# Performance work log

Hardware: AMD Instinct MI355X
Metric: run time of the kernel (lower is better)

## Reference

```python
import jax, jax.numpy as jnp
import numpy as np

B, T, D = 4, 512, 512
NB, NH, PF, K = 2, 8, 2, 4
INNER = PF * D          # 1024
DH = INNER // NH        # 128
NC = 1000
EPS = 1e-5


def _ln(x, s, b):
    mu = x.mean(-1, keepdims=True)
    var = x.var(-1, keepdims=True)
    return (x - mu) / jnp.sqrt(var + EPS) * s + b


def _causal_conv(x, k, b):
    # x: [B,T,C], depthwise kernel k: [C,K]
    kk = k.shape[-1]
    xp = jnp.pad(x, ((0, 0), (kk - 1, 0), (0, 0)))
    t = x.shape[1]
    y = sum(xp[:, j:j + t, :] * k[:, j] for j in range(kk))
    return y + b


def _mlstm_scan(q, k, v, ip, fp):
    # q,k,v: [B,T,NH,DH]; ip,fp: [B,T,NH]
    b, t, nh, dh = q.shape
    C0 = jnp.zeros((b, nh, dh, dh), q.dtype)
    n0 = jnp.zeros((b, nh, dh), q.dtype)
    m0 = jnp.zeros((b, nh), q.dtype)

    def step(carry, xs):
        C, n, m = carry
        qt, kt, vt, ipt, fpt = xs
        fl = jax.nn.log_sigmoid(fpt)
        m_new = jnp.maximum(fl + m, ipt)
        i = jnp.exp(ipt - m_new)
        f = jnp.exp(fl + m - m_new)
        C = f[..., None, None] * C + i[..., None, None] * (vt[..., :, None] * kt[..., None, :])
        n = f[..., None] * n + i[..., None] * kt
        denom = jnp.maximum(jnp.abs(jnp.einsum('bhd,bhd->bh', n, qt)), 1.0)
        h = jnp.einsum('bhij,bhj->bhi', C, qt) / denom[..., None]
        return (C, n, m_new), h

    tm = lambda a: jnp.swapaxes(a, 0, 1)  # time-major
    _, h = jax.lax.scan(step, (C0, n0, m0), (tm(q), tm(k), tm(v), tm(ip), tm(fp)))
    return jnp.swapaxes(h, 0, 1)  # [B,T,NH,DH]


def _block(x, ln_s, ln_b, w_up, b_up, conv_k, conv_b, w_q, w_k, w_v,
           w_ig, b_ig, w_fg, b_fg, hn_s, w_down, b_down):
    b, t, d = x.shape
    xn = _ln(x, ln_s, ln_b)
    up = xn @ w_up + b_up                       # [B,T,2*INNER]
    xu, z = up[..., :INNER], up[..., INNER:]
    xc = jax.nn.silu(_causal_conv(xu, conv_k, conv_b))
    q = (xc @ w_q).reshape(b, t, NH, DH)
    k = (xc @ w_k).reshape(b, t, NH, DH) * (DH ** -0.5)
    v = (xu @ w_v).reshape(b, t, NH, DH)
    ip = xc @ w_ig + b_ig                       # [B,T,NH]
    fp = xc @ w_fg + b_fg
    h = _mlstm_scan(q, k, v, ip, fp)            # [B,T,NH,DH]
    mu = h.mean(-1, keepdims=True)
    var = h.var(-1, keepdims=True)
    h = (h - mu) / jnp.sqrt(var + EPS) * hn_s   # per-head norm, hn_s: [NH,DH]
    h = h.reshape(b, t, INNER) * jax.nn.silu(z)
    return x + h @ w_down + b_down


def setup_inputs() -> dict:
    key = jax.random.key(0)
    ks = jax.random.split(key, 24)
    g = lambda i, sh, sc: jax.random.normal(ks[i], sh, jnp.float32) * sc
    inp = {
        'x': g(0, (B, T, D), 1.0),
        'cls_token': g(1, (1, 1, D), 0.02),
        'ln_s': jnp.ones((NB, D)), 'ln_b': jnp.zeros((NB, D)),
        'w_up': g(2, (NB, D, 2 * INNER), D ** -0.5), 'b_up': jnp.zeros((NB, 2 * INNER)),
        'conv_k': g(3, (NB, INNER, K), 0.3), 'conv_b': jnp.zeros((NB, INNER)),
        'w_q': g(4, (NB, INNER, INNER), INNER ** -0.5),
        'w_k': g(5, (NB, INNER, INNER), INNER ** -0.5),
        'w_v': g(6, (NB, INNER, INNER), INNER ** -0.5),
        'w_ig': g(7, (NB, INNER, NH), INNER ** -0.5), 'b_ig': jnp.zeros((NB, NH)),
        'w_fg': g(8, (NB, INNER, NH), INNER ** -0.5),
        'b_fg': jnp.full((NB, NH), 3.0),
        'hn_s': jnp.ones((NB, NH, DH)),
        'w_down': g(9, (NB, INNER, D), INNER ** -0.5), 'b_down': jnp.zeros((NB, D)),
        'fc_ln_s': jnp.ones((D,)), 'fc_ln_b': jnp.zeros((D,)),
        'fc_w': g(10, (D, NC), D ** -0.5), 'fc_b': jnp.zeros((NC,)),
    }
    return inp


def reference(x, cls_token, ln_s, ln_b, w_up, b_up, conv_k, conv_b, w_q, w_k, w_v,
              w_ig, b_ig, w_fg, b_fg, hn_s, w_down, b_down,
              fc_ln_s, fc_ln_b, fc_w, fc_b):
    b = x.shape[0]
    # append class token at the last position ('last')
    h = jnp.concatenate([x, jnp.broadcast_to(cls_token, (b, 1, x.shape[-1]))], axis=1)
    for i in range(NB):
        h = _block(h, ln_s[i], ln_b[i], w_up[i], b_up[i], conv_k[i], conv_b[i],
                   w_q[i], w_k[i], w_v[i], w_ig[i], b_ig[i], w_fg[i], b_fg[i],
                   hn_s[i], w_down[i], b_down[i])
    cls = h[:, -1, :]
    y = jax.nn.relu(_ln(cls, fc_ln_s, fc_ln_b)) @ fc_w + fc_b
    return y
```

## Files before the change

kernel.cpp:

```cpp
#include <hip/hip_runtime.h>

#define EPSV 1e-5f
constexpr int Bsz = 4, T0 = 512, Dm = 512, TT = 513, NHh = 8, KK = 4;
constexpr int IN = 1024, DHd = 128, NCc = 1000;
constexpr int ROWS = Bsz * TT;
constexpr int MPAD = 2176;
constexpr int NCH = 9;

constexpr size_t WT_UP = 0;
constexpr size_t WT_Q  = WT_UP + 2048 * 512;
constexpr size_t WT_K  = WT_Q + 1024 * 1024;
constexpr size_t WT_V  = WT_K + 1024 * 1024;
constexpr size_t WT_DN = WT_V + 1024 * 1024;
constexpr size_t WT_STRIDE = WT_DN + 512 * 1024;

typedef __attribute__((ext_vector_type(8))) short bf16x8;
typedef __attribute__((ext_vector_type(4))) float f32x4;
typedef __attribute__((ext_vector_type(4))) unsigned short ushort4v;
typedef __attribute__((ext_vector_type(8))) unsigned short ushort8v;
typedef unsigned short u16;

__device__ __forceinline__ float siluf(float x) { return x / (1.f + __expf(-x)); }
__device__ __forceinline__ u16 f2bf(float f) {
    unsigned int u = __float_as_uint(f);
    u = (u + 0x7FFFu + ((u >> 16) & 1u)) >> 16;
    return (u16)u;
}
__device__ __forceinline__ float bfu(u16 u) {
    return __uint_as_float(((unsigned int)u) << 16);
}
__device__ __forceinline__ void gload16(const u16* g, u16* l) {
    __builtin_amdgcn_global_load_lds(
        (const __attribute__((address_space(1))) void*)g,
        (__attribute__((address_space(3))) void*)l, 16, 0, 0);
}

__global__ __launch_bounds__(256) void concat_kernel(const float* __restrict__ x,
                                                     const float* __restrict__ cls,
                                                     float* __restrict__ h) {
    int idx = blockIdx.x * 256 + threadIdx.x;
    if (idx >= Bsz * TT * Dm) return;
    int d = idx & (Dm - 1);
    int bt = idx >> 9;
    int t = bt % TT, b = bt / TT;
    h[idx] = (t < T0) ? x[((size_t)(b * T0 + t)) * Dm + d] : cls[d];
}

__global__ __launch_bounds__(256) void ln_kernel(const float* __restrict__ in,
                                                 const float* __restrict__ s,
                                                 const float* __restrict__ bb,
                                                 u16* __restrict__ out16) {
    int row = blockIdx.x, tid = threadIdx.x;
    const float* r = in + (size_t)row * Dm;
    __shared__ float s1[4], s2[4];
    float x0 = r[tid], x1 = r[tid + 256];
    float sum = x0 + x1, sq = x0 * x0 + x1 * x1;
#pragma unroll
    for (int o = 32; o > 0; o >>= 1) { sum += __shfl_xor(sum, o); sq += __shfl_xor(sq, o); }
    if ((tid & 63) == 0) { s1[tid >> 6] = sum; s2[tid >> 6] = sq; }
    __syncthreads();
    sum = s1[0] + s1[1] + s1[2] + s1[3];
    sq  = s2[0] + s2[1] + s2[2] + s2[3];
    float mu = sum / Dm, var = sq / Dm - mu * mu, inv = rsqrtf(var + EPSV);
    out16[(size_t)row * Dm + tid]       = f2bf((x0 - mu) * inv * s[tid] + bb[tid]);
    out16[(size_t)row * Dm + tid + 256] = f2bf((x1 - mu) * inv * s[tid + 256] + bb[tid + 256]);
}

__global__ __launch_bounds__(256) void w_transpose_kernel(const float* __restrict__ wup,
        const float* __restrict__ wq, const float* __restrict__ wk,
        const float* __restrict__ wv, const float* __restrict__ wdn,
        u16* __restrict__ wt) {
    int y = blockIdx.y;
    int blk = y / 5, sel = y - blk * 5;
    int Kd, N; const float* src; size_t doff;
    if (sel == 0)      { Kd = 512;  N = 2048; src = wup + (size_t)blk * 512 * 2048; doff = WT_UP; }
    else if (sel == 1) { Kd = 1024; N = 1024; src = wq  + (size_t)blk * 1024 * 1024; doff = WT_Q; }
    else if (sel == 2) { Kd = 1024; N = 1024; src = wk  + (size_t)blk * 1024 * 1024; doff = WT_K; }
    else if (sel == 3) { Kd = 1024; N = 1024; src = wv  + (size_t)blk * 1024 * 1024; doff = WT_V; }
    else               { Kd = 1024; N = 512;  src = wdn + (size_t)blk * 1024 * 512;  doff = WT_DN; }
    u16* dst = wt + (size_t)blk * WT_STRIDE + doff;
    int ntx = N >> 5;
    int ntiles = ntx * (Kd >> 5);
    int ti = blockIdx.x;
    if (ti >= ntiles) return;
    int tk = ti / ntx, tn = ti - tk * ntx;
    __shared__ u16 s[32][33];
    int tx = threadIdx.x & 31, ty = threadIdx.x >> 5;
#pragma unroll
    for (int i = 0; i < 4; i++) {
        int k = tk * 32 + ty + i * 8;
        s[ty + i * 8][tx] = f2bf(src[(size_t)k * N + tn * 32 + tx]);
    }
    __syncthreads();
#pragma unroll
    for (int i = 0; i < 4; i++) {
        int n = tn * 32 + ty + i * 8;
        dst[(size_t)n * Kd + tk * 32 + tx] = s[tx][ty + i * 8];
    }
}

template<int BM, int BN>
__device__ __forceinline__ void gemm_tile_body(const u16* __restrict__ A, int lda,
                                               const u16* __restrict__ Wt, int Kd,
                                               const float* __restrict__ bias,
                                               const float* __restrict__ resid, int ldr,
                                               float* __restrict__ Cout, int ldc,
                                               int M, float scale, int m0, int n0,
                                               u16 (*As)[BM][40], u16 (*Bs)[BN][40]) {
    constexpr int MT = BM / 32;
    constexpr int NT = BN / 32;
    constexpr int ANV = BM / 64;
    constexpr int BNV = BN / 64;
    int tid = threadIdx.x;
    int wave = tid >> 6, lane = tid & 63;
    int wm = (wave >> 1) * (BM / 2), wn = (wave & 1) * (BN / 2);
    int lrow = lane & 15, lquad = lane >> 4;

    f32x4 acc[MT][NT];
#pragma unroll
    for (int i = 0; i < MT; i++)
#pragma unroll
        for (int j = 0; j < NT; j++)
#pragma unroll
            for (int r = 0; r < 4; r++) acc[i][j][r] = 0.f;

    int am, ak, bn, bk;
    if (BM == 128) { am = tid >> 1; ak = (tid & 1) * 16; }
    else           { am = tid >> 2; ak = (tid & 3) * 8; }
    if (BN == 128) { bn = tid & 127; bk = (tid >> 7) * 16; }
    else           { bn = tid & 63;  bk = (tid >> 6) * 8; }
    int gm = m0 + am;
    const u16* arow = A + (size_t)(gm < M ? gm : 0) * lda + ak;
    bool avalid = gm < M;
    const u16* wrow = Wt + (size_t)(n0 + bn) * Kd + bk;

    ushort8v areg[ANV];
    ushort8v breg[BNV];

    auto load_tile = [&](int k0) {
        if (avalid) {
#pragma unroll
            for (int i = 0; i < ANV; i++) areg[i] = *(const ushort8v*)(arow + k0 + i * 8);
        } else {
#pragma unroll
            for (int i = 0; i < ANV; i++) areg[i] = (ushort8v){0,0,0,0,0,0,0,0};
        }
#pragma unroll
        for (int i = 0; i < BNV; i++) breg[i] = *(const ushort8v*)(wrow + k0 + i * 8);
    };
    auto store_tile = [&](int buf) {
#pragma unroll
        for (int i = 0; i < ANV; i++)
            *(ushort8v*)&As[buf][am][ak + i * 8] = areg[i];
#pragma unroll
        for (int i = 0; i < BNV; i++)
            *(ushort8v*)&Bs[buf][bn][bk + i * 8] = breg[i];
    };

    load_tile(0);
    store_tile(0);
    __syncthreads();

    int nk = Kd >> 5;
#pragma unroll 1
    for (int it = 0; it < nk; it++) {
        int cur = it & 1;
        bool more = (it + 1 < nk);
        if (more) load_tile((it + 1) << 5);
        bf16x8 afr[MT], bfr[NT];
#pragma unroll
        for (int mt = 0; mt < MT; mt++)
            afr[mt] = *(const bf16x8*)&As[cur][wm + mt * 16 + lrow][lquad * 8];
#pragma unroll
        for (int nt = 0; nt < NT; nt++)
            bfr[nt] = *(const bf16x8*)&Bs[cur][wn + nt * 16 + lrow][lquad * 8];
#pragma unroll
        for (int mt = 0; mt < MT; mt++)
#pragma unroll
            for (int nt = 0; nt < NT; nt++)
                acc[mt][nt] = __builtin_amdgcn_mfma_f32_16x16x32_bf16(
                    afr[mt], bfr[nt], acc[mt][nt], 0, 0, 0);
        if (more) store_tile(cur ^ 1);
        __syncthreads();
    }

#pragma unroll
    for (int mt = 0; mt < MT; mt++) {
#pragma unroll
        for (int r = 0; r < 4; r++) {
            int gmr = m0 + wm + mt * 16 + lquad * 4 + r;
            if (gmr >= M) continue;
#pragma unroll
            for (int nt = 0; nt < NT; nt++) {
                int gn = n0 + wn + nt * 16 + lrow;
                float v = acc[mt][nt][r] * scale;
                if (bias) v += bias[gn];
                if (resid) v += resid[(size_t)gmr * ldr + gn];
                Cout[(size_t)gmr * ldc + gn] = v;
            }
        }
    }
}

template<int BM, int BN>
__global__ __launch_bounds__(256, 2) void gemm_mfma_kernel(const u16* __restrict__ A, int lda,
                                                           const u16* __restrict__ Wt, int Kd,
                                                           const float* __restrict__ bias,
                                                           const float* __restrict__ resid, int ldr,
                                                           float* __restrict__ Cout, int ldc,
                                                           int M, float scale) {
    __shared__ __align__(16) u16 As[2][BM][40];
    __shared__ __align__(16) u16 Bs[2][BN][40];
    gemm_tile_body<BM, BN>(A, lda, Wt, Kd, bias, resid, ldr, Cout, ldc, M, scale,
                           blockIdx.y * BM, blockIdx.x * BN, As, Bs);
}

__device__ __forceinline__ void gemm128_body(const u16* __restrict__ A, int lda,
                                             const u16* __restrict__ Wt, int Kd,
                                             const float* __restrict__ bias,
                                             float* __restrict__ Cout, int ldc,
                                             int M, float scale, int m0, int n0,
                                             u16* As, u16* Bs) {
    int tid = threadIdx.x;
    int wave = tid >> 6, lane = tid & 63;
    int lrow = lane & 15, lquad = lane >> 4;
    int wm = (wave >> 1) * 64, wn = (wave & 1) * 64;

    const u16* ag0 = A + (size_t)(m0 + wave * 16 + (lane >> 2)) * lda + (lane & 3) * 8;
    const u16* ag1 = ag0 + (size_t)64 * lda;
    const u16* bg0 = Wt + (size_t)(n0 + wave * 16 + (lane >> 2)) * Kd + (lane & 3) * 8;
    const u16* bg1 = bg0 + (size_t)64 * Kd;
    u16* la0 = As + wave * 512;
    u16* la1 = As + 2048 + wave * 512;
    u16* lb0 = Bs + wave * 512;
    u16* lb1 = Bs + 2048 + wave * 512;

    f32x4 acc[4][4];
#pragma unroll
    for (int i = 0; i < 4; i++)
#pragma unroll
        for (int j = 0; j < 4; j++)
#pragma unroll
            for (int r = 0; r < 4; r++) acc[i][j][r] = 0.f;

    int nk = Kd >> 5;
#pragma unroll 1
    for (int it = 0; it < nk; it++) {
        int k0 = it << 5;
        gload16(ag0 + k0, la0);
        gload16(ag1 + k0, la1);
        gload16(bg0 + k0, lb0);
        gload16(bg1 + k0, lb1);
        __syncthreads();
        bf16x8 afr[4], bfr[4];
#pragma unroll
        for (int mt = 0; mt < 4; mt++)
            afr[mt] = *(const bf16x8*)&As[(wm + mt * 16 + lrow) * 32 + lquad * 8];
#pragma unroll
        for (int nt = 0; nt < 4; nt++)
            bfr[nt] = *(const bf16x8*)&Bs[(wn + nt * 16 + lrow) * 32 + lquad * 8];
#pragma unroll
        for (int mt = 0; mt < 4; mt++)
#pragma unroll
            for (int nt = 0; nt < 4; nt++)
                acc[mt][nt] = __builtin_amdgcn_mfma_f32_16x16x32_bf16(
                    afr[mt], bfr[nt], acc[mt][nt], 0, 0, 0);
        __syncthreads();
    }

#pragma unroll
    for (int mt = 0; mt < 4; mt++) {
#pragma unroll
        for (int r = 0; r < 4; r++) {
            int gmr = m0 + wm + mt * 16 + lquad * 4 + r;
            if (gmr >= M) continue;
#pragma unroll
            for (int nt = 0; nt < 4; nt++) {
                int gn = n0 + wn + nt * 16 + lrow;
                float v = acc[mt][nt][r] * scale;
                if (bias) v += bias[gn];
                Cout[(size_t)gmr * ldc + gn] = v;
            }
        }
    }
}

__global__ __launch_bounds__(256, 2) void up_gl_kernel(const u16* __restrict__ A,
        const u16* __restrict__ Wt, const float* __restrict__ bias, float* __restrict__ C) {
    __shared__ __align__(16) u16 As[128 * 32];
    __shared__ __align__(16) u16 Bs[128 * 32];
    gemm128_body(A, Dm, Wt, Dm, bias, C, 2 * IN, ROWS, 1.f,
                 blockIdx.y * 128, blockIdx.x * 128, As, Bs);
}

__global__ __launch_bounds__(256, 2) void qkv_gl_kernel(const u16* __restrict__ xc16,
                                                        const u16* __restrict__ xu16,
                                                        const u16* __restrict__ wtblk,
                                                        float* __restrict__ fq,
                                                        float* __restrict__ fk,
                                                        float* __restrict__ fv,
                                                        float kscale) {
    __shared__ __align__(16) u16 As[128 * 32];
    __shared__ __align__(16) u16 Bs[128 * 32];
    int sel = blockIdx.x >> 3, nx = blockIdx.x & 7;
    const u16* A = (sel == 2) ? xu16 : xc16;
    const u16* Wt = wtblk + ((sel == 0) ? WT_Q : (sel == 1) ? WT_K : WT_V);
    float* C = (sel == 0) ? fq : (sel == 1) ? fk : fv;
    float scale = (sel == 1) ? kscale : 1.f;
    gemm128_body(A, IN, Wt, IN, nullptr, C, IN, ROWS, scale,
                 blockIdx.y * 128, nx * 128, As, Bs);
}

__global__ __launch_bounds__(256) void conv_silu_kernel(const float* __restrict__ up,
                                                        const float* __restrict__ ck,
                                                        const float* __restrict__ cb,
                                                        float* __restrict__ xc,
                                                        u16* __restrict__ xc16,
                                                        u16* __restrict__ xu16) {
    int idx = blockIdx.x * 256 + threadIdx.x;
    if (idx >= ROWS * IN) return;
    int c = idx & (IN - 1);
    int bt = idx >> 10;
    int t = bt % TT, b = bt / TT;
    float cur = up[((size_t)(b * TT + t)) * (2 * IN) + c];
    float acc = cb[c] + cur * ck[c * KK + (KK - 1)];
#pragma unroll
    for (int j = 0; j < KK - 1; j++) {
        int tt = t - (KK - 1) + j;
        if (tt >= 0) acc += up[((size_t)(b * TT + tt)) * (2 * IN) + c] * ck[c * KK + j];
    }
    float s = siluf(acc);
    xc[idx] = s;
    xc16[idx] = f2bf(s);
    xu16[idx] = f2bf(cur);
}

__global__ __launch_bounds__(256) void gate_w_transpose(const float* __restrict__ wig,
                                                        const float* __restrict__ wfg,
                                                        float* __restrict__ wt) {
    int idx = blockIdx.x * 256 + threadIdx.x;
    int k = idx & 1023;
    int g = (idx >> 10) & 15;
    int blk = idx >> 14;
    const float* w = (g < 8) ? (wig + (size_t)blk * IN * NHh) : (wfg + (size_t)blk * IN * NHh);
    wt[idx] = w[k * NHh + (g & 7)];
}

__global__ __launch_bounds__(256) void gates_kernel(const float* __restrict__ xc,
                                                    const float* __restrict__ wt,
                                                    const float* __restrict__ big,
                                                    const float* __restrict__ bfg,
                                                    float* __restrict__ ip, float* __restrict__ fp) {
    int row = blockIdx.x, tid = threadIdx.x;
    __shared__ float sx[IN];
    *(float4*)&sx[tid * 4] = *(const float4*)(xc + (size_t)row * IN + tid * 4);
    __syncthreads();
    int g = tid >> 4, l = tid & 15;
    const float* wrow = wt + g * IN;
    float acc = 0.f;
#pragma unroll
    for (int j = 0; j < 16; j++) {
        int k = j * 64 + l * 4;
        float4 w4 = *(const float4*)(wrow + k);
        float4 x4 = *(const float4*)&sx[k];
        acc += w4.x * x4.x + w4.y * x4.y + w4.z * x4.z + w4.w * x4.w;
    }
#pragma unroll
    for (int o = 8; o > 0; o >>= 1) acc += __shfl_down(acc, o, 16);
    if (l == 0) {
        if (g < 8) ip[(size_t)row * NHh + g] = acc + big[g];
        else       fp[(size_t)row * NHh + (g - 8)] = acc + bfg[g - 8];
    }
}

__global__ __launch_bounds__(64) void gate_scan_kernel(const float* __restrict__ ip,
        const float* __restrict__ fp, float* __restrict__ gG, float* __restrict__ gM,
        float* __restrict__ gMb, float* __restrict__ gDec) {
    constexpr int PER = 9;
    int chain = blockIdx.x;
    int b = chain >> 3, h = chain & 7;
    int lane = threadIdx.x;
    int tbase = lane * PER;
    float lcs[PER];
    float gi[PER];
    float csum = 0.f;
#pragma unroll
    for (int i = 0; i < PER; i++) {
        int t = tbase + i;
        float fpv = 0.f, ipv = 0.f;
        if (t < TT) {
            size_t gidx = (size_t)(b * TT + t) * NHh + h;
            fpv = fp[gidx]; ipv = ip[gidx];
        }
        float flv = (fpv >= 0.f) ? -log1pf(__expf(-fpv)) : (fpv - log1pf(__expf(fpv)));
        if (t >= TT) flv = 0.f;
        csum += flv;
        lcs[i] = csum;
        gi[i] = ipv;
    }
    float ps = csum;
#pragma unroll
    for (int o = 1; o < 64; o <<= 1) {
        float v = __shfl_up(ps, o);
        if (lane >= o) ps += v;
    }
    float Fexcl = ps - csum;
    float G[PER];
    float cmax = -1e30f;
#pragma unroll
    for (int i = 0; i < PER; i++) {
        int t = tbase + i;
        G[i] = (t < TT) ? (gi[i] - (Fexcl + lcs[i])) : -1e30f;
        cmax = fmaxf(cmax, G[i]);
        lcs[i] = cmax;
    }
    float pm = cmax;
#pragma unroll
    for (int o = 1; o < 64; o <<= 1) {
        float v = __shfl_up(pm, o);
        if (lane >= o) pm = fmaxf(pm, v);
    }
    float Me = __shfl_up(pm, 1);
    if (lane == 0) Me = -1e30f;
    __shared__ float sMb[NCH];
#pragma unroll
    for (int i = 0; i < PER; i++) {
        int t = tbase + i;
        if (t < TT) {
            float Mt = fmaxf(0.f, fmaxf(Me, lcs[i]));
            gG[chain * TT + t] = G[i];
            gM[chain * TT + t] = Mt;
            if (((t & 63) == 63) || t == TT - 1) sMb[t >> 6] = Mt;
        }
    }
    __syncthreads();
    if (lane < NCH) {
        float Mb = sMb[lane];
        float Mbp = (lane == 0) ? 0.f : sMb[lane - 1];
        gMb[chain * NCH + lane] = Mb;
        gDec[chain * NCH + lane] = __expf(Mbp - Mb);
    }
}

__global__ __launch_bounds__(256, 2) void chunk_state_kernel(const float* __restrict__ kk,
        const float* __restrict__ vv, const float* __restrict__ gG,
        const float* __restrict__ gMb, float* __restrict__ P, float* __restrict__ nP) {
    int c = blockIdx.x, chain = blockIdx.y;
    int b = chain >> 3, h = chain & 7;
    int t0 = c * 64;
    int nvalid = min(64, TT - t0);
    __shared__ __align__(16) u16 sWv[128][72];
    __shared__ __align__(16) u16 sKt[128][72];
    __shared__ float sw[64];
    int tid = threadIdx.x;
    if (tid < 64) {
        float Mb = gMb[chain * NCH + c];
        sw[tid] = (tid < nvalid) ? __expf(gG[chain * TT + t0 + tid] - Mb) : 0.f;
    }
    __syncthreads();

    {
        int j = tid >> 2, d0 = (tid & 3) * 32;
        bool val = j < nvalid;
        float wj = sw[j];
        size_t gb = ((size_t)(b * TT + t0 + j)) * IN + h * DHd + d0;
#pragma unroll
        for (int i = 0; i < 8; i++) {
            float4 k4 = val ? *(const float4*)(kk + gb + i * 4) : make_float4(0.f, 0.f, 0.f, 0.f);
            float4 v4 = val ? *(const float4*)(vv + gb + i * 4) : make_float4(0.f, 0.f, 0.f, 0.f);
            int dd = d0 + i * 4;
            int jc = j ^ (((dd >> 5) & 3) << 4);
            sKt[dd + 0][jc] = f2bf(k4.x);
            sKt[dd + 1][jc] = f2bf(k4.y);
            sKt[dd + 2][jc] = f2bf(k4.z);
            sKt[dd + 3][jc] = f2bf(k4.w);
            sWv[dd + 0][jc] = f2bf(v4.x * wj);
            sWv[dd + 1][jc] = f2bf(v4.y * wj);
            sWv[dd + 2][jc] = f2bf(v4.z * wj);
            sWv[dd + 3][jc] = f2bf(v4.w * wj);
        }
    }
    __syncthreads();

    int wave = tid >> 6, lane = tid & 63;
    int lrow = lane & 15, lquad = lane >> 4;
    int wm = (wave >> 1) * 64, wn = (wave & 1) * 64;
    f32x4 acc[4][4];
#pragma unroll
    for (int mt = 0; mt < 4; mt++)
#pragma unroll
        for (int nt = 0; nt < 4; nt++)
#pragma unroll
            for (int r = 0; r < 4; r++) acc[mt][nt][r] = 0.f;

#pragma unroll
    for (int ks = 0; ks < 2; ks++) {
        bf16x8 af[4], bfr[4];
#pragma unroll
        for (int mt = 0; mt < 4; mt++) {
            int r = wm + mt * 16 + lrow;
            int g = (ks * 4 + lquad) ^ (((r >> 5) & 3) << 1);
            af[mt] = *(const bf16x8*)&sWv[r][g * 8];
        }
#pragma unroll
        for (int nt = 0; nt < 4; nt++) {
            int r = wn + nt * 16 + lrow;
            int g = (ks * 4 + lquad) ^ (((r >> 5) & 3) << 1);
            bfr[nt] = *(const bf16x8*)&sKt[r][g * 8];
        }
#pragma unroll
        for (int mt = 0; mt < 4; mt++)
#pragma unroll
            for (int nt = 0; nt < 4; nt++)
                acc[mt][nt] = __builtin_amdgcn_mfma_f32_16x16x32_bf16(
                    af[mt], bfr[nt], acc[mt][nt], 0, 0, 0);
    }

    float* Pbase = P + (((size_t)(c * 32 + chain)) << 14);
#pragma unroll
    for (int mt = 0; mt < 4; mt++)
#pragma unroll
        for (int r = 0; r < 4; r++) {
            int e = wm + mt * 16 + lquad * 4 + r;
#pragma unroll
            for (int nt = 0; nt < 4; nt++) {
                int d = wn + nt * 16 + lrow;
                Pbase[(size_t)e * 128 + d] = acc[mt][nt][r];
            }
        }

    {
        int d = tid >> 1, jh = (tid & 1) * 32;
        int swz = ((d >> 5) & 3) << 4;
        float an = 0.f;
#pragma unroll
        for (int j = 0; j < 32; j++) {
            int jj = jh + j;
            an += sw[jj] * bfu(sKt[d][jj ^ swz]);
        }
        an += __shfl_xor(an, 1);
        if ((tid & 1) == 0) nP[(size_t)(c * 32 + chain) * 128 + d] = an;
    }
}

__global__ __launch_bounds__(256) void chunk_combine_kernel(float* __restrict__ P,
        const float* __restrict__ gDec) {
    int chain = blockIdx.x >> 6;
    int idx = (blockIdx.x & 63) * 256 + threadIdx.x;
    float run = 0.f;
    for (int c = 0; c < NCH; c++) {
        size_t a = (((size_t)(c * 32 + chain)) << 14) + idx;
        float tmp = P[a];
        P[a] = run;
        run = run * gDec[chain * NCH + c] + tmp;
    }
}

__global__ __launch_bounds__(256) void n_combine_kernel(float* __restrict__ nP,
        const float* __restrict__ gDec) {
    int gidx = blockIdx.x * 256 + threadIdx.x;
    int chain = gidx >> 7, d = gidx & 127;
    float run = 0.f;
    for (int c = 0; c < NCH; c++) {
        size_t a = (size_t)(c * 32 + chain) * 128 + d;
        float tmp = nP[a];
        nP[a] = run;
        run = run * gDec[chain * NCH + c] + tmp;
    }
}

__global__ __launch_bounds__(512, 2) void chunk_out_kernel(const float* __restrict__ qq,
        const float* __restrict__ kk, const float* __restrict__ vv,
        const float* __restrict__ gG, const float* __restrict__ gM,
        const float* __restrict__ gMb, const float* __restrict__ P,
        const float* __restrict__ nP, float* __restrict__ hs) {
    int c = blockIdx.x, chain = blockIdx.y;
    int b = chain >> 3, h = chain & 7;
    int t0 = c * 64;
    int nvalid = min(64, TT - t0);
    __shared__ __align__(16) u16 smem[30720];
    __shared__ float sG[64], sM[64], sWr[64], sInv[64], sNb[128], sRS[2][64];
    u16* sQ  = smem;
    u16* sCB = smem + 8704;
    u16* sK  = smem + 8704;
    u16* sVt = smem;
    u16* sD  = smem + 26112;
    int tid = threadIdx.x;
    int wave = tid >> 6, lane = tid & 63;
    int lrow = lane & 15, lquad = lane >> 4;
    int mq = wave >> 1, nh = wave & 1;

    float Mbprev = (c > 0) ? gMb[chain * NCH + c - 1] : 0.f;
    if (tid < 64) {
        bool val = tid < nvalid;
        sG[tid] = val ? gG[chain * TT + t0 + tid] : -1e30f;
        float Mv = val ? gM[chain * TT + t0 + tid] : 1e30f;
        sM[tid] = Mv;
        sWr[tid] = val ? __expf(Mbprev - Mv) : 0.f;
    }
    if (tid >= 128 && tid < 256) sNb[tid - 128] = nP[(size_t)(c * 32 + chain) * 128 + (tid - 128)];

    {
        int lr = tid >> 3, c0 = (tid & 7) * 16;
        bool val = lr < nvalid;
        size_t gb = ((size_t)(b * TT + t0 + lr)) * IN + h * DHd + c0;
#pragma unroll
        for (int i = 0; i < 4; i++) {
            float4 q4 = val ? *(const float4*)(qq + gb + i * 4) : make_float4(0.f,0.f,0.f,0.f);
            ushort4v tq = {f2bf(q4.x), f2bf(q4.y), f2bf(q4.z), f2bf(q4.w)};
            *(ushort4v*)&sQ[lr * 136 + c0 + i * 4] = tq;
        }
    }
    {
        const float* CBbase = P + (((size_t)(c * 32 + chain)) << 14);
        int e = tid >> 2, d0 = (tid & 3) * 32;
#pragma unroll
        for (int i = 0; i < 8; i++) {
            float4 c4 = *(const float4*)(CBbase + (size_t)e * 128 + d0 + i * 4);
            ushort4v tc = {f2bf(c4.x), f2bf(c4.y), f2bf(c4.z), f2bf(c4.w)};
            *(ushort4v*)&sCB[e * 136 + d0 + i * 4] = tc;
        }
    }
    __syncthreads();

    f32x4 acc[4];
#pragma unroll
    for (int tt = 0; tt < 4; tt++)
#pragma unroll
        for (int r = 0; r < 4; r++) acc[tt][r] = 0.f;
#pragma unroll 1
    for (int ks = 0; ks < 4; ks++) {
        bf16x8 af = *(const bf16x8*)&sQ[(mq * 16 + lrow) * 136 + ks * 32 + lquad * 8];
#pragma unroll
        for (int tt = 0; tt < 4; tt++) {
            bf16x8 bf = *(const bf16x8*)&sCB[(nh * 64 + tt * 16 + lrow) * 136 + ks * 32 + lquad * 8];
            acc[tt] = __builtin_amdgcn_mfma_f32_16x16x32_bf16(af, bf, acc[tt], 0, 0, 0);
        }
    }
#pragma unroll
    for (int tt = 0; tt < 4; tt++)
#pragma unroll
        for (int r = 0; r < 4; r++) acc[tt][r] *= sWr[mq * 16 + lquad * 4 + r];
    __syncthreads();

    {
        int lr = tid >> 3, c0 = (tid & 7) * 16;
        bool val = lr < nvalid;
        size_t gb = ((size_t)(b * TT + t0 + lr)) * IN + h * DHd + c0;
#pragma unroll
        for (int i = 0; i < 4; i++) {
            float4 k4 = val ? *(const float4*)(kk + gb + i * 4) : make_float4(0.f,0.f,0.f,0.f);
            ushort4v tk = {f2bf(k4.x), f2bf(k4.y), f2bf(k4.z), f2bf(k4.w)};
            *(ushort4v*)&sK[lr * 136 + c0 + i * 4] = tk;
        }
    }
    __syncthreads();

    {
        f32x4 accS[2];
#pragma unroll
        for (int tt = 0; tt < 2; tt++)
#pragma unroll
            for (int r = 0; r < 4; r++) accS[tt][r] = 0.f;
#pragma unroll 1
        for (int ks = 0; ks < 4; ks++) {
            bf16x8 af = *(const bf16x8*)&sQ[(mq * 16 + lrow) * 136 + ks * 32 + lquad * 8];
#pragma unroll
            for (int tt = 0; tt < 2; tt++) {
                bf16x8 bf = *(const bf16x8*)&sK[((nh * 2 + tt) * 16 + lrow) * 136 + ks * 32 + lquad * 8];
                accS[tt] = __builtin_amdgcn_mfma_f32_16x16x32_bf16(af, bf, accS[tt], 0, 0, 0);
            }
        }
        float rsum[4] = {0.f, 0.f, 0.f, 0.f};
#pragma unroll
        for (int tt = 0; tt < 2; tt++) {
            int j = (nh * 2 + tt) * 16 + lrow;
            float Gj = sG[j];
#pragma unroll
            for (int r = 0; r < 4; r++) {
                int t = mq * 16 + lquad * 4 + r;
                float w = (j <= t) ? __expf(Gj - sM[t]) : 0.f;
                float wD = accS[tt][r] * w;
                rsum[r] += wD;
                sD[t * 72 + j] = f2bf(wD);
            }
        }
#pragma unroll
        for (int r = 0; r < 4; r++) {
#pragma unroll
            for (int msk = 1; msk < 16; msk <<= 1) rsum[r] += __shfl_xor(rsum[r], msk);
        }
        if (lrow == 0) {
#pragma unroll
            for (int r = 0; r < 4; r++) sRS[nh][mq * 16 + lquad * 4 + r] = rsum[r];
        }
    }
    __syncthreads();

    if (tid < 64) {
        float qn = 0.f;
#pragma unroll 1
        for (int d4 = 0; d4 < 32; d4++) {
            ushort4v q4 = *(const ushort4v*)&sQ[tid * 136 + d4 * 4];
            float4 nb = *(const float4*)&sNb[d4 * 4];
            qn += bfu(q4.x) * nb.x + bfu(q4.y) * nb.y + bfu(q4.z) * nb.z + bfu(q4.w) * nb.w;
        }
        float den = sRS[0][tid] + sRS[1][tid] + sWr[tid] * qn;
        sInv[tid] = 1.f / fmaxf(fabsf(den), 1.f);
    }
    __syncthreads();

    {
        int e = tid & 127, tg = (tid >> 7) * 16;
#pragma unroll 1
        for (int i = 0; i < 16; i++) {
            int t = tg + i;
            float v = (t < nvalid) ? vv[((size_t)(b * TT + t0 + t)) * IN + h * DHd + e] : 0.f;
            sVt[e * 72 + t] = f2bf(v);
        }
    }
    __syncthreads();

#pragma unroll 1
    for (int ks = 0; ks < 2; ks++) {
        bf16x8 af = *(const bf16x8*)&sD[(mq * 16 + lrow) * 72 + ks * 32 + lquad * 8];
#pragma unroll
        for (int tt = 0; tt < 4; tt++) {
            bf16x8 bf = *(const bf16x8*)&sVt[(nh * 64 + tt * 16 + lrow) * 72 + ks * 32 + lquad * 8];
            acc[tt] = __builtin_amdgcn_mfma_f32_16x16x32_bf16(af, bf, acc[tt], 0, 0, 0);
        }
    }

#pragma unroll
    for (int tt = 0; tt < 4; tt++) {
#pragma unroll
        for (int r = 0; r < 4; r++) {
            int t = mq * 16 + lquad * 4 + r;
            if (t < nvalid) {
                int e = nh * 64 + tt * 16 + lrow;
                hs[((size_t)(b * TT + t0 + t)) * IN + h * DHd + e] = acc[tt][r] * sInv[t];
            }
        }
    }
}

__global__ __launch_bounds__(64) void headnorm_kernel(const float* __restrict__ hs,
                                                      const float* __restrict__ hn,
                                                      const float* __restrict__ up,
                                                      u16* __restrict__ out16) {
    int idx = blockIdx.x;
    int h = idx & 7, bt = idx >> 3;
    int tid = threadIdx.x;
    size_t base = (size_t)bt * IN + h * DHd;
    float x0 = hs[base + tid], x1 = hs[base + 64 + tid];
    float sum = x0 + x1, sq = x0 * x0 + x1 * x1;
#pragma unroll
    for (int o = 32; o > 0; o >>= 1) { sum += __shfl_xor(sum, o); sq += __shfl_xor(sq, o); }
    float mu = sum / DHd, var = sq / DHd - mu * mu, inv = rsqrtf(var + EPSV);
    size_t zb = (size_t)bt * (2 * IN) + IN + h * DHd;
    out16[base + tid]      = f2bf((x0 - mu) * inv * hn[h * DHd + tid]      * siluf(up[zb + tid]));
    out16[base + 64 + tid] = f2bf((x1 - mu) * inv * hn[h * DHd + 64 + tid] * siluf(up[zb + 64 + tid]));
}

__global__ __launch_bounds__(256) void cls_ln_kernel(const float* __restrict__ hbuf,
                                                     const float* __restrict__ s, const float* __restrict__ bb,
                                                     float* __restrict__ vcls) {
    int b = blockIdx.x, tid = threadIdx.x;
    const float* r = hbuf + ((size_t)b * TT + TT - 1) * Dm;
    __shared__ float s1[4], s2[4];
    float x0 = r[tid], x1 = r[tid + 256];
    float sum = x0 + x1, sq = x0 * x0 + x1 * x1;
#pragma unroll
    for (int o = 32; o > 0; o >>= 1) { sum += __shfl_xor(sum, o); sq += __shfl_xor(sq, o); }
    if ((tid & 63) == 0) { s1[tid >> 6] = sum; s2[tid >> 6] = sq; }
    __syncthreads();
    sum = s1[0] + s1[1] + s1[2] + s1[3];
    sq  = s2[0] + s2[1] + s2[2] + s2[3];
    float mu = sum / Dm, var = sq / Dm - mu * mu, inv = rsqrtf(var + EPSV);
    float n0 = (x0 - mu) * inv * s[tid] + bb[tid];
    float n1 = (x1 - mu) * inv * s[tid + 256] + bb[tid + 256];
    vcls[b * Dm + tid]       = fmaxf(n0, 0.f);
    vcls[b * Dm + tid + 256] = fmaxf(n1, 0.f);
}

__global__ __launch_bounds__(256) void fc_kernel(const float* __restrict__ vcls,
                                                 const float* __restrict__ fw,
                                                 const float* __restrict__ fb,
                                                 float* __restrict__ out) {
    __shared__ float svc[Bsz][Dm];
    __shared__ float sred[4][256];
    int tid = threadIdx.x;
    int j0 = blockIdx.x * 64;
    {
        const float4* src = (const float4*)vcls;
        float4* dst = (float4*)&svc[0][0];
        dst[tid] = src[tid];
        dst[tid + 256] = src[tid + 256];
    }
    __syncthreads();
    int j = j0 + (tid & 63);
    int chunk = tid >> 6;
    int kbase = chunk * 128;
    float a0 = 0.f, a1 = 0.f, a2 = 0.f, a3 = 0.f;
    if (j < NCc) {
        const float* fwp = fw + (size_t)kbase * NCc + j;
#pragma unroll 4
        for (int kk = 0; kk < 128; kk++) {
            float w = fwp[(size_t)kk * NCc];
            a0 += svc[0][kbase + kk] * w;
            a1 += svc[1][kbase + kk] * w;
            a2 += svc[2][kbase + kk] * w;
            a3 += svc[3][kbase + kk] * w;
        }
    }
    int jl = tid & 63;
    sred[chunk][jl * 4 + 0] = a0;
    sred[chunk][jl * 4 + 1] = a1;
    sred[chunk][jl * 4 + 2] = a2;
    sred[chunk][jl * 4 + 3] = a3;
    __syncthreads();
    if (tid < 64) {
        int jj = j0 + tid;
        if (jj < NCc) {
            float bias = fb[jj];
#pragma unroll
            for (int b = 0; b < Bsz; b++) {
                float v = sred[0][tid * 4 + b] + sred[1][tid * 4 + b]
                        + sred[2][tid * 4 + b] + sred[3][tid * 4 + b];
                out[b * NCc + jj] = v + bias;
            }
        }
    }
}

extern "C" void kernel_launch(void* const* d_in, const int* in_sizes, int n_in,
                              void* d_out, int out_size, void* d_ws, size_t ws_size,
                              hipStream_t stream) {
    const float* x      = (const float*)d_in[0];
    const float* cls    = (const float*)d_in[1];
    const float* ln_s   = (const float*)d_in[2];
    const float* ln_b   = (const float*)d_in[3];
    const float* w_up   = (const float*)d_in[4];
    const float* b_up   = (const float*)d_in[5];
    const float* conv_k = (const float*)d_in[6];
    const float* conv_b = (const float*)d_in[7];
    const float* w_q    = (const float*)d_in[8];
    const float* w_k    = (const float*)d_in[9];
    const float* w_v    = (const float*)d_in[10];
    const float* w_ig   = (const float*)d_in[11];
    const float* b_ig   = (const float*)d_in[12];
    const float* w_fg   = (const float*)d_in[13];
    const float* b_fg   = (const float*)d_in[14];
    const float* hn_s   = (const float*)d_in[15];
    const float* w_down = (const float*)d_in[16];
    const float* b_down = (const float*)d_in[17];
    const float* fcls   = (const float*)d_in[18];
    const float* fclb   = (const float*)d_in[19];
    const float* fc_w   = (const float*)d_in[20];
    const float* fc_b   = (const float*)d_in[21];
    float* out = (float*)d_out;

    float* ws = (float*)d_ws;
    size_t off = 0;
    float* f_h  = ws + off; off += (size_t)ROWS * Dm;
    float* f_up = ws + off; off += (size_t)ROWS * 2 * IN;
    float* f_xc = ws + off; off += (size_t)ROWS * IN;
    float* f_q  = ws + off; off += (size_t)ROWS * IN;
    float* f_k  = ws + off; off += (size_t)ROWS * IN;
    float* f_v  = ws + off; off += (size_t)ROWS * IN;
    float* f_hs = ws + off; off += (size_t)ROWS * IN;
    float* f_ip = ws + off; off += (size_t)ROWS * NHh;
    float* f_fp = ws + off; off += (size_t)ROWS * NHh;
    float* g_G  = ws + off; off += 32 * TT;
    float* g_M  = ws + off; off += 32 * TT;
    float* g_Mb = ws + off; off += 32 * NCH;
    float* g_De = ws + off; off += 32 * NCH;
    float* g_P  = ws + off; off += (size_t)NCH * 32 * DHd * DHd;
    float* g_nP = ws + off; off += (size_t)NCH * 32 * DHd;
    float* f_vc = ws + off; off += Bsz * Dm;
    float* g_wt = ws + off; off += 2 * 16 * IN;
    u16* g_Wt  = (u16*)(ws + off); off += (2 * WT_STRIDE + 1) / 2;
    u16* f_xn16 = (u16*)(ws + off); off += ((size_t)MPAD * Dm) / 2;
    u16* f_xc16 = (u16*)(ws + off); off += ((size_t)MPAD * IN) / 2;
    u16* f_xu16 = (u16*)(ws + off); off += ((size_t)MPAD * IN) / 2;
    u16* f_xg16 = (u16*)(ws + off); off += ((size_t)ROWS * IN + 1) / 2;

    const float kscale = 0.08838834764831845f;
    const int MB = (ROWS + 127) / 128;
    const int MB64 = (ROWS + 63) / 64;

    concat_kernel<<<(ROWS * Dm + 255) / 256, 256, 0, stream>>>(x, cls, f_h);
    gate_w_transpose<<<(2 * 16 * IN + 255) / 256, 256, 0, stream>>>(w_ig, w_fg, g_wt);
    w_transpose_kernel<<<dim3(1024, 10), 256, 0, stream>>>(w_up, w_q, w_k, w_v, w_down, g_Wt);

    for (int blk = 0; blk < 2; blk++) {
        const float* p_ln_s = ln_s + blk * Dm;
        const float* p_ln_b = ln_b + blk * Dm;
        const float* p_bup  = b_up + (size_t)blk * 2 * IN;
        const float* p_ck   = conv_k + (size_t)blk * IN * KK;
        const float* p_cb   = conv_b + (size_t)blk * IN;
        const float* p_big  = b_ig + (size_t)blk * NHh;
        const float* p_bfg  = b_fg + (size_t)blk * NHh;
        const float* p_hns  = hn_s + (size_t)blk * NHh * DHd;
        const float* p_bd   = b_down + (size_t)blk * Dm;
        const u16*   p_wt   = g_Wt + (size_t)blk * WT_STRIDE;

        ln_kernel<<<ROWS, 256, 0, stream>>>(f_h, p_ln_s, p_ln_b, f_xn16);

        up_gl_kernel<<<dim3(2 * IN / 128, MB), 256, 0, stream>>>(
            f_xn16, p_wt + WT_UP, p_bup, f_up);

        conv_silu_kernel<<<(ROWS * IN + 255) / 256, 256, 0, stream>>>(
            f_up, p_ck, p_cb, f_xc, f_xc16, f_xu16);

        qkv_gl_kernel<<<dim3(24, MB), 256, 0, stream>>>(
            f_xc16, f_xu16, p_wt, f_q, f_k, f_v, kscale);

        gates_kernel<<<ROWS, 256, 0, stream>>>(f_xc, g_wt + blk * 16 * IN, p_big, p_bfg,
                                               f_ip, f_fp);

        gate_scan_kernel<<<32, 64, 0, stream>>>(f_ip, f_fp, g_G, g_M, g_Mb, g_De);
        chunk_state_kernel<<<dim3(NCH, 32), 256, 0, stream>>>(f_k, f_v, g_G, g_Mb, g_P, g_nP);
        chunk_combine_kernel<<<32 * 64, 256, 0, stream>>>(g_P, g_De);
        n_combine_kernel<<<16, 256, 0, stream>>>(g_nP, g_De);
        chunk_out_kernel<<<dim3(NCH, 32), 512, 0, stream>>>(f_q, f_k, f_v, g_G, g_M, g_Mb,
                                                            g_P, g_nP, f_hs);

        headnorm_kernel<<<ROWS * NHh, 64, 0, stream>>>(f_hs, p_hns, f_up, f_xg16);

        gemm_mfma_kernel<64, 64><<<dim3(Dm / 64, MB64), 256, 0, stream>>>(
            f_xg16, IN, p_wt + WT_DN, IN, p_bd, f_h, Dm, f_h, Dm, ROWS, 1.f);
    }

    cls_ln_kernel<<<Bsz, 256, 0, stream>>>(f_h, fcls, fclb, f_vc);
    fc_kernel<<<(NCc + 63) / 64, 256, 0, stream>>>(f_vc, fc_w, fc_b, out);
}
```

Measured before the change: 451.6 us.

## Fuse conv with gates, headnorm into chunk output, cls LN into FC

Merges the causal-conv/SiLU kernel with the gate projection so the fp32 xc buffer is no longer written or read. Head normalisation and the z-gating are moved into the epilogue of chunk_out through shared memory, which removes the fp32 hs round trip and one launch. The chunk combine now writes the carried state as bf16, halving the reads in chunk_out, and absorbs the n combine. The class-token LayerNorm is folded into the FC kernel. Together these cut several launches and a large amount of global memory traffic, in exchange for more register and shared-memory pressure in the fused kernels.

```diff
diff --git a/kernel.cpp b/kernel.cpp
--- a/kernel.cpp
+++ b/kernel.cpp
@@ -311,50 +311,40 @@
                  blockIdx.y * 128, nx * 128, As, Bs);
 }
 
-__global__ __launch_bounds__(256) void conv_silu_kernel(const float* __restrict__ up,
-                                                        const float* __restrict__ ck,
-                                                        const float* __restrict__ cb,
-                                                        float* __restrict__ xc,
-                                                        u16* __restrict__ xc16,
-                                                        u16* __restrict__ xu16) {
-    int idx = blockIdx.x * 256 + threadIdx.x;
-    if (idx >= ROWS * IN) return;
-    int c = idx & (IN - 1);
-    int bt = idx >> 10;
-    int t = bt % TT, b = bt / TT;
-    float cur = up[((size_t)(b * TT + t)) * (2 * IN) + c];
-    float acc = cb[c] + cur * ck[c * KK + (KK - 1)];
+__global__ __launch_bounds__(256) void convgates_kernel(const float* __restrict__ up,
+        const float* __restrict__ ck, const float* __restrict__ cb,
+        const float* __restrict__ wt, const float* __restrict__ big,
+        const float* __restrict__ bfg,
+        u16* __restrict__ xc16, u16* __restrict__ xu16,
+        float* __restrict__ ip, float* __restrict__ fp) {
+    int row = blockIdx.x, tid = threadIdx.x;
+    int b = row / TT, t = row - b * TT;
+    __shared__ float sx[IN];
+    int c0 = tid * 4;
+    float4 cur = *(const float4*)(up + (size_t)row * (2 * IN) + c0);
+    float a0 = cb[c0 + 0] + cur.x * ck[(c0 + 0) * KK + 3];
+    float a1 = cb[c0 + 1] + cur.y * ck[(c0 + 1) * KK + 3];
+    float a2 = cb[c0 + 2] + cur.z * ck[(c0 + 2) * KK + 3];
+    float a3 = cb[c0 + 3] + cur.w * ck[(c0 + 3) * KK + 3];
 #pragma unroll
     for (int j = 0; j < KK - 1; j++) {
-        int tt = t - (KK - 1) + j;
-        if (tt >= 0) acc += up[((size_t)(b * TT + tt)) * (2 * IN) + c] * ck[c * KK + j];
-    }
-    float s = siluf(acc);
-    xc[idx] = s;
-    xc16[idx] = f2bf(s);
-    xu16[idx] = f2bf(cur);
-}
-
-__global__ __launch_bounds__(256) void gate_w_transpose(const float* __restrict__ wig,
-                                                        const float* __restrict__ wfg,
-                                                        float* __restrict__ wt) {
-    int idx = blockIdx.x * 256 + threadIdx.x;
-    int k = idx & 1023;
-    int g = (idx >> 10) & 15;
-    int blk = idx >> 14;
-    const float* w = (g < 8) ? (wig + (size_t)blk * IN * NHh) : (wfg + (size_t)blk * IN * NHh);
-    wt[idx] = w[k * NHh + (g & 7)];
-}
-
-__global__ __launch_bounds__(256) void gates_kernel(const float* __restrict__ xc,
-                                                    const float* __restrict__ wt,
-                                                    const float* __restrict__ big,
-                                                    const float* __restrict__ bfg,
-                                                    float* __restrict__ ip, float* __restrict__ fp) {
-    int row = blockIdx.x, tid = threadIdx.x;
-    __shared__ float sx[IN];
-    *(float4*)&sx[tid * 4] = *(const float4*)(xc + (size_t)row * IN + tid * 4);
-    __syncthreads();
+        int tt2 = t - (KK - 1) + j;
+        if (tt2 >= 0) {
+            float4 pv = *(const float4*)(up + ((size_t)(b * TT + tt2)) * (2 * IN) + c0);
+            a0 += pv.x * ck[(c0 + 0) * KK + j];
+            a1 += pv.y * ck[(c0 + 1) * KK + j];
+            a2 += pv.z * ck[(c0 + 2) * KK + j];
+            a3 += pv.w * ck[(c0 + 3) * KK + j];
+        }
+    }
+    float s0 = siluf(a0), s1v = siluf(a1), s2v = siluf(a2), s3v = siluf(a3);
+    *(float4*)&sx[c0] = make_float4(s0, s1v, s2v, s3v);
+    ushort4v xc4 = {f2bf(s0), f2bf(s1v), f2bf(s2v), f2bf(s3v)};
+    *(ushort4v*)&xc16[(size_t)row * IN + c0] = xc4;
+    ushort4v xu4 = {f2bf(cur.x), f2bf(cur.y), f2bf(cur.z), f2bf(cur.w)};
+    *(ushort4v*)&xu16[(size_t)row * IN + c0] = xu4;
+    __syncthreads();
+
     int g = tid >> 4, l = tid & 15;
     const float* wrow = wt + g * IN;
     float acc = 0.f;
@@ -543,37 +533,36 @@
     }
 }
 
-__global__ __launch_bounds__(256) void chunk_combine_kernel(float* __restrict__ P,
-        const float* __restrict__ gDec) {
+__global__ __launch_bounds__(256) void chunk_combine_kernel(const float* __restrict__ P,
+        u16* __restrict__ CB, float* __restrict__ nP, const float* __restrict__ gDec) {
     int chain = blockIdx.x >> 6;
-    int idx = (blockIdx.x & 63) * 256 + threadIdx.x;
+    int seg = blockIdx.x & 63;
+    int idx = seg * 256 + threadIdx.x;
     float run = 0.f;
     for (int c = 0; c < NCH; c++) {
         size_t a = (((size_t)(c * 32 + chain)) << 14) + idx;
         float tmp = P[a];
-        P[a] = run;
+        CB[a] = f2bf(run);
         run = run * gDec[chain * NCH + c] + tmp;
     }
-}
-
-__global__ __launch_bounds__(256) void n_combine_kernel(float* __restrict__ nP,
-        const float* __restrict__ gDec) {
-    int gidx = blockIdx.x * 256 + threadIdx.x;
-    int chain = gidx >> 7, d = gidx & 127;
-    float run = 0.f;
-    for (int c = 0; c < NCH; c++) {
-        size_t a = (size_t)(c * 32 + chain) * 128 + d;
-        float tmp = nP[a];
-        nP[a] = run;
-        run = run * gDec[chain * NCH + c] + tmp;
+    if (seg == 0 && threadIdx.x < 128) {
+        int d = threadIdx.x;
+        float rn = 0.f;
+        for (int c = 0; c < NCH; c++) {
+            size_t a = (size_t)(c * 32 + chain) * 128 + d;
+            float tmp = nP[a];
+            nP[a] = rn;
+            rn = rn * gDec[chain * NCH + c] + tmp;
+        }
     }
 }
 
 __global__ __launch_bounds__(512, 2) void chunk_out_kernel(const float* __restrict__ qq,
         const float* __restrict__ kk, const float* __restrict__ vv,
         const float* __restrict__ gG, const float* __restrict__ gM,
-        const float* __restrict__ gMb, const float* __restrict__ P,
-        const float* __restrict__ nP, float* __restrict__ hs) {
+        const float* __restrict__ gMb, const u16* __restrict__ CB,
+        const float* __restrict__ nP, const float* __restrict__ hn,
+        const float* __restrict__ up, u16* __restrict__ out16) {
     int c = blockIdx.x, chain = blockIdx.y;
     int b = chain >> 3, h = chain & 7;
     int t0 = c * 64;
@@ -585,6 +574,7 @@
     u16* sK  = smem + 8704;
     u16* sVt = smem;
     u16* sD  = smem + 26112;
+    float* hv = (float*)smem;
     int tid = threadIdx.x;
     int wave = tid >> 6, lane = tid & 63;
     int lrow = lane & 15, lquad = lane >> 4;
@@ -612,14 +602,12 @@
         }
     }
     {
-        const float* CBbase = P + (((size_t)(c * 32 + chain)) << 14);
+        const u16* CBbase = CB + (((size_t)(c * 32 + chain)) << 14);
         int e = tid >> 2, d0 = (tid & 3) * 32;
 #pragma unroll
-        for (int i = 0; i < 8; i++) {
-            float4 c4 = *(const float4*)(CBbase + (size_t)e * 128 + d0 + i * 4);
-            ushort4v tc = {f2bf(c4.x), f2bf(c4.y), f2bf(c4.z), f2bf(c4.w)};
-            *(ushort4v*)&sCB[e * 136 + d0 + i * 4] = tc;
-        }
+        for (int i = 0; i < 4; i++)
+            *(ushort8v*)&sCB[e * 136 + d0 + i * 8] =
+                *(const ushort8v*)(CBbase + (size_t)e * 128 + d0 + i * 8);
     }
     __syncthreads();
 
@@ -731,59 +719,45 @@
         }
     }
 
+    __syncthreads();
 #pragma unroll
     for (int tt = 0; tt < 4; tt++) {
 #pragma unroll
         for (int r = 0; r < 4; r++) {
             int t = mq * 16 + lquad * 4 + r;
-            if (t < nvalid) {
-                int e = nh * 64 + tt * 16 + lrow;
-                hs[((size_t)(b * TT + t0 + t)) * IN + h * DHd + e] = acc[tt][r] * sInv[t];
+            int e = nh * 64 + tt * 16 + lrow;
+            hv[t * 132 + e] = acc[tt][r] * sInv[t];
+        }
+    }
+    __syncthreads();
+    {
+        int t = tid >> 3, s = tid & 7;
+        float vals[16];
+        float sum = 0.f, sq = 0.f;
+#pragma unroll
+        for (int i = 0; i < 16; i++) {
+            float v = hv[t * 132 + s * 16 + i];
+            vals[i] = v; sum += v; sq += v * v;
+        }
+#pragma unroll
+        for (int m = 1; m < 8; m <<= 1) { sum += __shfl_xor(sum, m); sq += __shfl_xor(sq, m); }
+        float mu = sum / DHd, var = sq / DHd - mu * mu, inv2 = rsqrtf(var + EPSV);
+        if (t < nvalid) {
+            size_t bt = (size_t)(b * TT + t0 + t);
+            const float* zp = up + bt * (2 * IN) + IN + h * DHd + s * 16;
+            u16* op = out16 + bt * IN + h * DHd + s * 16;
+#pragma unroll
+            for (int i = 0; i < 16; i++) {
+                float hnv = hn[h * DHd + s * 16 + i];
+                op[i] = f2bf((vals[i] - mu) * inv2 * hnv * siluf(zp[i]));
             }
         }
     }
 }
 
-__global__ __launch_bounds__(64) void headnorm_kernel(const float* __restrict__ hs,
-                                                      const float* __restrict__ hn,
-                                                      const float* __restrict__ up,
-                                                      u16* __restrict__ out16) {
-    int idx = blockIdx.x;
-    int h = idx & 7, bt = idx >> 3;
-    int tid = threadIdx.x;
-    size_t base = (size_t)bt * IN + h * DHd;
-    float x0 = hs[base + tid], x1 = hs[base + 64 + tid];
-    float sum = x0 + x1, sq = x0 * x0 + x1 * x1;
-#pragma unroll
-    for (int o = 32; o > 0; o >>= 1) { sum += __shfl_xor(sum, o); sq += __shfl_xor(sq, o); }
-    float mu = sum / DHd, var = sq / DHd - mu * mu, inv = rsqrtf(var + EPSV);
-    size_t zb = (size_t)bt * (2 * IN) + IN + h * DHd;
-    out16[base + tid]      = f2bf((x0 - mu) * inv * hn[h * DHd + tid]      * siluf(up[zb + tid]));
-    out16[base + 64 + tid] = f2bf((x1 - mu) * inv * hn[h * DHd + 64 + tid] * siluf(up[zb + 64 + tid]));
-}
-
-__global__ __launch_bounds__(256) void cls_ln_kernel(const float* __restrict__ hbuf,
-                                                     const float* __restrict__ s, const float* __restrict__ bb,
-                                                     float* __restrict__ vcls) {
-    int b = blockIdx.x, tid = threadIdx.x;
-    const float* r = hbuf + ((size_t)b * TT + TT - 1) * Dm;
-    __shared__ float s1[4], s2[4];
-    float x0 = r[tid], x1 = r[tid + 256];
-    float sum = x0 + x1, sq = x0 * x0 + x1 * x1;
-#pragma unroll
-    for (int o = 32; o > 0; o >>= 1) { sum += __shfl_xor(sum, o); sq += __shfl_xor(sq, o); }
-    if ((tid & 63) == 0) { s1[tid >> 6] = sum; s2[tid >> 6] = sq; }
-    __syncthreads();
-    sum = s1[0] + s1[1] + s1[2] + s1[3];
-    sq  = s2[0] + s2[1] + s2[2] + s2[3];
-    float mu = sum / Dm, var = sq / Dm - mu * mu, inv = rsqrtf(var + EPSV);
-    float n0 = (x0 - mu) * inv * s[tid] + bb[tid];
-    float n1 = (x1 - mu) * inv * s[tid + 256] + bb[tid + 256];
-    vcls[b * Dm + tid]       = fmaxf(n0, 0.f);
-    vcls[b * Dm + tid + 256] = fmaxf(n1, 0.f);
-}
-
-__global__ __launch_bounds__(256) void fc_kernel(const float* __restrict__ vcls,
+__global__ __launch_bounds__(256) void fc_kernel(const float* __restrict__ hbuf,
+                                                 const float* __restrict__ fcls,
+                                                 const float* __restrict__ fclb,
                                                  const float* __restrict__ fw,
                                                  const float* __restrict__ fb,
                                                  float* __restrict__ out) {
@@ -792,10 +766,23 @@
     int tid = threadIdx.x;
     int j0 = blockIdx.x * 64;
     {
-        const float4* src = (const float4*)vcls;
-        float4* dst = (float4*)&svc[0][0];
-        dst[tid] = src[tid];
-        dst[tid + 256] = src[tid + 256];
+        int r = tid >> 6, lane = tid & 63;
+        const float* hrow = hbuf + ((size_t)r * TT + TT - 1) * Dm;
+        float v[8];
+        float sum = 0.f, sq = 0.f;
+#pragma unroll
+        for (int k = 0; k < 8; k++) {
+            v[k] = hrow[lane + k * 64];
+            sum += v[k]; sq += v[k] * v[k];
+        }
+#pragma unroll
+        for (int o = 32; o > 0; o >>= 1) { sum += __shfl_xor(sum, o); sq += __shfl_xor(sq, o); }
+        float mu = sum / Dm, var = sq / Dm - mu * mu, inv = rsqrtf(var + EPSV);
+#pragma unroll
+        for (int k = 0; k < 8; k++) {
+            int e = lane + k * 64;
+            svc[r][e] = fmaxf((v[k] - mu) * inv * fcls[e] + fclb[e], 0.f);
+        }
     }
     __syncthreads();
     int j = j0 + (tid & 63);
@@ -831,6 +818,17 @@
             }
         }
     }
+}
+
+__global__ __launch_bounds__(256) void gate_w_transpose(const float* __restrict__ wig,
+                                                        const float* __restrict__ wfg,
+                                                        float* __restrict__ wt) {
+    int idx = blockIdx.x * 256 + threadIdx.x;
+    int k = idx & 1023;
+    int g = (idx >> 10) & 15;
+    int blk = idx >> 14;
+    const float* w = (g < 8) ? (wig + (size_t)blk * IN * NHh) : (wfg + (size_t)blk * IN * NHh);
+    wt[idx] = w[k * NHh + (g & 7)];
 }
 
 extern "C" void kernel_launch(void* const* d_in, const int* in_sizes, int n_in,
@@ -864,11 +862,9 @@
     size_t off = 0;
     float* f_h  = ws + off; off += (size_t)ROWS * Dm;
     float* f_up = ws + off; off += (size_t)ROWS * 2 * IN;
-    float* f_xc = ws + off; off += (size_t)ROWS * IN;
     float* f_q  = ws + off; off += (size_t)ROWS * IN;
     float* f_k  = ws + off; off += (size_t)ROWS * IN;
     float* f_v  = ws + off; off += (size_t)ROWS * IN;
-    float* f_hs = ws + off; off += (size_t)ROWS * IN;
     float* f_ip = ws + off; off += (size_t)ROWS * NHh;
     float* f_fp = ws + off; off += (size_t)ROWS * NHh;
     float* g_G  = ws + off; off += 32 * TT;
@@ -877,8 +873,8 @@
     float* g_De = ws + off; off += 32 * NCH;
     float* g_P  = ws + off; off += (size_t)NCH * 32 * DHd * DHd;
     float* g_nP = ws + off; off += (size_t)NCH * 32 * DHd;
-    float* f_vc = ws + off; off += Bsz * Dm;
     float* g_wt = ws + off; off += 2 * 16 * IN;
+    u16* g_CB  = (u16*)(ws + off); off += ((size_t)NCH * 32 * DHd * DHd + 1) / 2;
     u16* g_Wt  = (u16*)(ws + off); off += (2 * WT_STRIDE + 1) / 2;
     u16* f_xn16 = (u16*)(ws + off); off += ((size_t)MPAD * Dm) / 2;
     u16* f_xc16 = (u16*)(ws + off); off += ((size_t)MPAD * IN) / 2;
@@ -910,28 +906,22 @@
         up_gl_kernel<<<dim3(2 * IN / 128, MB), 256, 0, stream>>>(
             f_xn16, p_wt + WT_UP, p_bup, f_up);
 
-        conv_silu_kernel<<<(ROWS * IN + 255) / 256, 256, 0, stream>>>(
-            f_up, p_ck, p_cb, f_xc, f_xc16, f_xu16);
+        convgates_kernel<<<ROWS, 256, 0, stream>>>(
+            f_up, p_ck, p_cb, g_wt + blk * 16 * IN, p_big, p_bfg,
+            f_xc16, f_xu16, f_ip, f_fp);
 
         qkv_gl_kernel<<<dim3(24, MB), 256, 0, stream>>>(
             f_xc16, f_xu16, p_wt, f_q, f_k, f_v, kscale);
 
-        gates_kernel<<<ROWS, 256, 0, stream>>>(f_xc, g_wt + blk * 16 * IN, p_big, p_bfg,
-                                               f_ip, f_fp);
-
         gate_scan_kernel<<<32, 64, 0, stream>>>(f_ip, f_fp, g_G, g_M, g_Mb, g_De);
         chunk_state_kernel<<<dim3(NCH, 32), 256, 0, stream>>>(f_k, f_v, g_G, g_Mb, g_P, g_nP);
-        chunk_combine_kernel<<<32 * 64, 256, 0, stream>>>(g_P, g_De);
-        n_combine_kernel<<<16, 256, 0, stream>>>(g_nP, g_De);
+        chunk_combine_kernel<<<32 * 64, 256, 0, stream>>>(g_P, g_CB, g_nP, g_De);
         chunk_out_kernel<<<dim3(NCH, 32), 512, 0, stream>>>(f_q, f_k, f_v, g_G, g_M, g_Mb,
-                                                            g_P, g_nP, f_hs);
-
-        headnorm_kernel<<<ROWS * NHh, 64, 0, stream>>>(f_hs, p_hns, f_up, f_xg16);
+                                                            g_CB, g_nP, p_hns, f_up, f_xg16);
 
         gemm_mfma_kernel<64, 64><<<dim3(Dm / 64, MB64), 256, 0, stream>>>(
             f_xg16, IN, p_wt + WT_DN, IN, p_bd, f_h, Dm, f_h, Dm, ROWS, 1.f);
     }
 
-    cls_ln_kernel<<<Bsz, 256, 0, stream>>>(f_h, fcls, fclb, f_vc);
-    fc_kernel<<<(NCc + 63) / 64, 256, 0, stream>>>(f_vc, fc_w, fc_b, out);
-}
+    fc_kernel<<<(NCc + 63) / 64, 256, 0, stream>>>(f_h, fcls, fclb, fc_w, fc_b, out);
+}
```

Result: faster. 435.4 us (-3.6%).
